# Kernel tuning notes

Hardware: AMD Instinct MI355X
Metric: run time of the kernel (lower is better)

## Reference

```python
import jax, jax.numpy as jnp
import numpy as np

N, E, H = 50000, 800000, 4
IN, HID, OUT = 128, 64, 16
SIM_THRESH = 0.1
NEG_SLOPE = 0.01  # F.leaky_relu default


def setup_inputs() -> dict:
    key = jax.random.key(0)
    k = jax.random.split(key, 6)
    x = jax.random.normal(k[0], (N, IN), jnp.float32)
    row = jax.random.randint(k[1], (E,), 0, N)
    col = jax.random.randint(k[2], (E,), 0, N)
    W0 = jax.random.normal(k[3], (H, IN, HID), jnp.float32) / np.float32(np.sqrt(IN))
    W1 = jax.random.normal(k[4], (H, H * HID, HID), jnp.float32) / np.float32(np.sqrt(H * HID))
    W2 = jax.random.normal(k[5], (1, H * HID, OUT), jnp.float32) / np.float32(np.sqrt(H * HID))
    return {"x": x, "W0": W0, "W1": W1, "W2": W2, "row": row, "col": col}


def _att_coef(x, row, col):
    # cosine similarity on edges only (honors the sparse edge structure)
    nrm = jnp.linalg.norm(x, axis=1, keepdims=True)
    xn = x / jnp.maximum(nrm, 1e-12)
    sim = jnp.sum(xn[row] * xn[col], axis=1)            # [E]
    sim = jnp.where(sim < SIM_THRESH, 0.0, sim)
    # L1 row-normalize the thresholded attention matrix
    rowsum = jax.ops.segment_sum(jnp.abs(sim), row, num_segments=N)
    rs_e = rowsum[row]
    att = jnp.where(rs_e > 0, sim / jnp.where(rs_e > 0, rs_e, 1.0), 0.0)
    # degree-based self-loop weight lam = 1/(deg+1), then exp of all nonzeros
    deg = jax.ops.segment_sum((att != 0).astype(x.dtype), row, num_segments=N)
    w_edge = jnp.where(att != 0, jnp.exp(att), 0.0)     # zero entries stay zero (dropped nnz)
    w_self = jnp.exp(1.0 / (deg + 1.0))                 # [N]
    return w_edge, w_self


def _layer(x, W, row, col, act):
    w_edge, w_self = _att_coef(x, row, col)
    z = jnp.einsum('nd,hdo->nho', x, W)                 # per-head projection
    msg = w_edge[:, None, None] * z[col]                # [E,h,o] gather + weight
    agg = jax.ops.segment_sum(msg, row, num_segments=N) + w_self[:, None, None] * z
    out = agg.reshape(N, -1)                            # concat heads (flatten(1))
    return jax.nn.leaky_relu(out, NEG_SLOPE) if act else out


def reference(x, W0, W1, W2, row, col):
    h = _layer(x, W0, row, col, True)
    h = _layer(h, W1, row, col, True)
    h = _layer(h, W2, row, col, False)
    return h
```

## Files before the change

### kernel.cpp

```cpp
#include <hip/hip_runtime.h>
#include <math.h>


static inline int cdiv(int a, int b){ return (a + b - 1) / b; }


__device__ inline float vdot(float4 a, float4 b){ return a.x*b.x + a.y*b.y + a.z*b.z + a.w*b.w; }
__device__ inline void vfma(float4& acc, float w, float4 b){
  acc.x += w*b.x; acc.y += w*b.y; acc.z += w*b.z; acc.w += w*b.w;
}
__device__ inline float4 vscale(float w, float4 a){ return make_float4(w*a.x, w*a.y, w*a.z, w*a.w); }

__device__ inline float wred(float d){
  #pragma unroll
  for (int off = 32; off; off >>= 1) d += __shfl_xor(d, off);
  return d;
}

__device__ inline unsigned short f2bf(float f){
  unsigned int u = __float_as_uint(f);
  unsigned int r = (u + 0x7FFFu + ((u >> 16) & 1u)) >> 16;
  return (unsigned short)r;
}
__device__ inline float bf2f(unsigned int us){ return __uint_as_float(us << 16); }

__device__ inline void bf8_to_f(uint4 v, float* f){
  f[0] = bf2f(v.x & 0xFFFFu); f[1] = bf2f(v.x >> 16);
  f[2] = bf2f(v.y & 0xFFFFu); f[3] = bf2f(v.y >> 16);
  f[4] = bf2f(v.z & 0xFFFFu); f[5] = bf2f(v.z >> 16);
  f[6] = bf2f(v.w & 0xFFFFu); f[7] = bf2f(v.w >> 16);
}


__global__ void count_kernel(const int* __restrict__ row, int* __restrict__ cnt, int E){
  int e = blockIdx.x * blockDim.x + threadIdx.x;
  if (e < E) atomicAdd(&cnt[row[e]], 1);
}

__global__ void scan1_kernel(const int* __restrict__ cnt, int* __restrict__ offs,
                             int* __restrict__ bsum, int n){
  __shared__ int tmp[256];
  int tid = threadIdx.x;
  int g = blockIdx.x * 256 + tid;
  int v = (g < n) ? cnt[g] : 0;
  tmp[tid] = v;
  __syncthreads();
  for (int off = 1; off < 256; off <<= 1){
    int t = (tid >= off) ? tmp[tid - off] : 0;
    __syncthreads();
    tmp[tid] += t;
    __syncthreads();
  }
  if (g < n) offs[g] = tmp[tid] - v;
  if (tid == 255) bsum[blockIdx.x] = tmp[255];
}

__global__ void scan2_kernel(int* __restrict__ bsum, int* __restrict__ offs, int nb, int n){
  __shared__ int tmp[256];
  int tid = threadIdx.x;
  int v = (tid < nb) ? bsum[tid] : 0;
  tmp[tid] = v;
  __syncthreads();
  for (int off = 1; off < 256; off <<= 1){
    int t = (tid >= off) ? tmp[tid - off] : 0;
    __syncthreads();
    tmp[tid] += t;
    __syncthreads();
  }
  if (tid < nb) bsum[tid] = tmp[tid] - v;
  if (tid == 255) offs[n] = tmp[255];
}

__global__ void scan3_kernel(int* __restrict__ offs, int* __restrict__ cur,
                             const int* __restrict__ bsum, int n){
  int g = blockIdx.x * 256 + threadIdx.x;
  if (g < n){
    int o = offs[g] + bsum[blockIdx.x];
    offs[g] = o;
    cur[g]  = o;
  }
}

__global__ void scatter_kernel(const int* __restrict__ row, const int* __restrict__ col,
                               int* __restrict__ cur, int* __restrict__ ecol, int E){
  int e = blockIdx.x * blockDim.x + threadIdx.x;
  if (e < E){
    int p = atomicAdd(&cur[row[e]], 1);
    ecol[p] = col[e];
  }
}


__global__ void invnorm128_kernel(const float* __restrict__ x, float* __restrict__ invn, int N){
  int n = blockIdx.x * 4 + (threadIdx.x >> 6);
  int lane = threadIdx.x & 63;
  if (n >= N) return;
  float2 a = ((const float2*)(x + (size_t)n * 128))[lane];
  float ss = a.x * a.x + a.y * a.y;
  ss = wred(ss);
  if (lane == 0) invn[n] = 1.0f / fmaxf(sqrtf(ss), 1e-12f);
}


template<int R>
__global__ void att_agg_wave128(const float* __restrict__ x, const float* __restrict__ invn,
                                const int* __restrict__ offs, const int* __restrict__ ecol,
                                float* __restrict__ out, int N){
  constexpr int LT = 64;
  __shared__ float tls[4][LT];
  __shared__ int   tlk[4][LT];
  const int wid  = threadIdx.x >> 6;
  const int lane = threadIdx.x & 63;
  const int half = lane >> 5, hl = lane & 31;
  const int hidx = wid * 2 + half;
  const int n = blockIdx.x * 2 + wid;
  if (n >= N) return;
  const int s = offs[n], e = offs[n + 1];
  const float inr = invn[n];
  const float4* xv = (const float4*)x;
  float4 a = xv[(size_t)n * 32 + hl];

  float4 br[R];
  float  simv[R];
  float  rowsum = 0.0f;
  int    deg = 0;

  #pragma unroll
  for (int r = 0; r < R; r++){
    simv[r] = 0.0f;
    int k = s + 2 * r + half;
    if (k < e){
      int c = ecol[k];
      float4 b = xv[(size_t)c * 32 + hl];
      br[r] = b;
      float d = vdot(a, b);
      #pragma unroll
      for (int off = 16; off; off >>= 1) d += __shfl_xor(d, off);
      d *= inr * invn[c];
      if (d < 0.1f) d = 0.0f;
      simv[r] = d;
      rowsum += d;
      deg += (d != 0.0f) ? 1 : 0;
    }
  }

  int tc = 0, kover = e;
  int k = s + 2 * R + half;
  for (; k + 2 < e; k += 4){
    int c0 = ecol[k], c1 = ecol[k + 2];
    float4 b0 = xv[(size_t)c0 * 32 + hl];
    float4 b1 = xv[(size_t)c1 * 32 + hl];
    float d0 = vdot(a, b0), d1 = vdot(a, b1);
    #pragma unroll
    for (int off = 16; off; off >>= 1){ d0 += __shfl_xor(d0, off); d1 += __shfl_xor(d1, off); }
    d0 *= inr * invn[c0];
    d1 *= inr * invn[c1];
    if (d0 < 0.1f) d0 = 0.0f;
    if (d1 < 0.1f) d1 = 0.0f;
    rowsum += d0 + d1;
    deg += (d0 != 0.0f) + (d1 != 0.0f);
    if (d0 > 0.0f){
      if (tc < LT){ if (hl == 0){ tls[hidx][tc] = d0; tlk[hidx][tc] = c0; } tc++; }
      else if (kover > k) kover = k;
    }
    if (d1 > 0.0f){
      if (tc < LT){ if (hl == 0){ tls[hidx][tc] = d1; tlk[hidx][tc] = c1; } tc++; }
      else if (kover > k + 2) kover = k + 2;
    }
  }
  if (k < e){
    int c0 = ecol[k];
    float4 b0 = xv[(size_t)c0 * 32 + hl];
    float d0 = vdot(a, b0);
    #pragma unroll
    for (int off = 16; off; off >>= 1) d0 += __shfl_xor(d0, off);
    d0 *= inr * invn[c0];
    if (d0 < 0.1f) d0 = 0.0f;
    rowsum += d0;
    deg += (d0 != 0.0f) ? 1 : 0;
    if (d0 > 0.0f){
      if (tc < LT){ if (hl == 0){ tls[hidx][tc] = d0; tlk[hidx][tc] = c0; } tc++; }
      else if (kover > k) kover = k;
    }
  }

  rowsum += __shfl_xor(rowsum, 32);
  deg    += __shfl_xor(deg, 32);
  const float invrs = (rowsum > 0.0f) ? 1.0f / rowsum : 0.0f;
  const float wself = expf(1.0f / (float)(deg + 1));

  float4 acc = (half == 0) ? vscale(wself, a) : make_float4(0.f, 0.f, 0.f, 0.f);
  #pragma unroll
  for (int r = 0; r < R; r++){
    if (simv[r] > 0.0f) vfma(acc, expf(simv[r] * invrs), br[r]);
  }
  int j = 0;
  for (; j + 1 < tc; j += 2){
    float w0 = expf(tls[hidx][j] * invrs);
    float w1 = expf(tls[hidx][j + 1] * invrs);
    int c0 = tlk[hidx][j], c1 = tlk[hidx][j + 1];
    float4 b0 = xv[(size_t)c0 * 32 + hl];
    float4 b1 = xv[(size_t)c1 * 32 + hl];
    vfma(acc, w0, b0);
    vfma(acc, w1, b1);
  }
  if (j < tc){
    float w0 = expf(tls[hidx][j] * invrs);
    float4 b0 = xv[(size_t)tlk[hidx][j] * 32 + hl];
    vfma(acc, w0, b0);
  }
  for (int k2 = kover; k2 < e; k2 += 2){
    int c = ecol[k2];
    float4 b = xv[(size_t)c * 32 + hl];
    float d = vdot(a, b);
    #pragma unroll
    for (int off = 16; off; off >>= 1) d += __shfl_xor(d, off);
    d *= inr * invn[c];
    if (d >= 0.1f) vfma(acc, expf(d * invrs), b);
  }

  acc.x += __shfl_xor(acc.x, 32);
  acc.y += __shfl_xor(acc.y, 32);
  acc.z += __shfl_xor(acc.z, 32);
  acc.w += __shfl_xor(acc.w, 32);
  if (half == 0) ((float4*)out)[(size_t)n * 32 + hl] = acc;
}


template<int R>
__global__ void att256_bf(const unsigned short* __restrict__ hbf,
                          const float* __restrict__ invn,
                          const int* __restrict__ offs, const int* __restrict__ ecol,
                          float* __restrict__ out, int N){
  constexpr int LT = 64;
  __shared__ float tls[4][LT];
  __shared__ int   tlk[4][LT];
  const int wid  = threadIdx.x >> 6;
  const int lane = threadIdx.x & 63;
  const int half = lane >> 5, hl = lane & 31;
  const int hidx = wid * 2 + half;
  const int n = blockIdx.x * 2 + wid;
  if (n >= N) return;
  const int s = offs[n], e = offs[n + 1];
  const float inr = invn[n];
  const uint4* hb = (const uint4*)hbf;

  float a8[8];
  bf8_to_f(hb[(size_t)n * 32 + hl], a8);

  uint4 brv[R];
  float simv[R];
  float rowsum = 0.0f;
  int   deg = 0;

  #pragma unroll
  for (int r = 0; r < R; r++){
    simv[r] = 0.0f;
    int k = s + 2 * r + half;
    if (k < e){
      int c = ecol[k];
      uint4 v = hb[(size_t)c * 32 + hl];
      brv[r] = v;
      float b8[8]; bf8_to_f(v, b8);
      float d = 0.0f;
      #pragma unroll
      for (int t = 0; t < 8; t++) d += a8[t] * b8[t];
      #pragma unroll
      for (int off = 16; off; off >>= 1) d += __shfl_xor(d, off);
      d *= inr * invn[c];
      if (d < 0.1f) d = 0.0f;
      simv[r] = d;
      rowsum += d;
      deg += (d != 0.0f) ? 1 : 0;
    }
  }

  int tc = 0, kover = e;
  int k = s + 2 * R + half;
  for (; k + 2 < e; k += 4){
    int c0 = ecol[k], c1 = ecol[k + 2];
    uint4 v0 = hb[(size_t)c0 * 32 + hl];
    uint4 v1 = hb[(size_t)c1 * 32 + hl];
    float b0[8], b1[8];
    bf8_to_f(v0, b0);
    bf8_to_f(v1, b1);
    float d0 = 0.0f, d1 = 0.0f;
    #pragma unroll
    for (int t = 0; t < 8; t++){ d0 += a8[t] * b0[t]; d1 += a8[t] * b1[t]; }
    #pragma unroll
    for (int off = 16; off; off >>= 1){ d0 += __shfl_xor(d0, off); d1 += __shfl_xor(d1, off); }
    d0 *= inr * invn[c0];
    d1 *= inr * invn[c1];
    if (d0 < 0.1f) d0 = 0.0f;
    if (d1 < 0.1f) d1 = 0.0f;
    rowsum += d0 + d1;
    deg += (d0 != 0.0f) + (d1 != 0.0f);
    if (d0 > 0.0f){
      if (tc < LT){ if (hl == 0){ tls[hidx][tc] = d0; tlk[hidx][tc] = c0; } tc++; }
      else if (kover > k) kover = k;
    }
    if (d1 > 0.0f){
      if (tc < LT){ if (hl == 0){ tls[hidx][tc] = d1; tlk[hidx][tc] = c1; } tc++; }
      else if (kover > k + 2) kover = k + 2;
    }
  }
  if (k < e){
    int c0 = ecol[k];
    uint4 v0 = hb[(size_t)c0 * 32 + hl];
    float b0[8]; bf8_to_f(v0, b0);
    float d0 = 0.0f;
    #pragma unroll
    for (int t = 0; t < 8; t++) d0 += a8[t] * b0[t];
    #pragma unroll
    for (int off = 16; off; off >>= 1) d0 += __shfl_xor(d0, off);
    d0 *= inr * invn[c0];
    if (d0 < 0.1f) d0 = 0.0f;
    rowsum += d0;
    deg += (d0 != 0.0f) ? 1 : 0;
    if (d0 > 0.0f){
      if (tc < LT){ if (hl == 0){ tls[hidx][tc] = d0; tlk[hidx][tc] = c0; } tc++; }
      else if (kover > k) kover = k;
    }
  }

  rowsum += __shfl_xor(rowsum, 32);
  deg    += __shfl_xor(deg, 32);
  const float invrs = (rowsum > 0.0f) ? 1.0f / rowsum : 0.0f;
  const float wself = expf(1.0f / (float)(deg + 1));

  float acc8[8];
  #pragma unroll
  for (int t = 0; t < 8; t++) acc8[t] = (half == 0) ? wself * a8[t] : 0.0f;
  #pragma unroll
  for (int r = 0; r < R; r++){
    if (simv[r] > 0.0f){
      float w = expf(simv[r] * invrs);
      float b8[8]; bf8_to_f(brv[r], b8);
      #pragma unroll
      for (int t = 0; t < 8; t++) acc8[t] += w * b8[t];
    }
  }
  int j = 0;
  for (; j + 1 < tc; j += 2){
    float w0 = expf(tls[hidx][j] * invrs);
    float w1 = expf(tls[hidx][j + 1] * invrs);
    uint4 v0 = hb[(size_t)tlk[hidx][j] * 32 + hl];
    uint4 v1 = hb[(size_t)tlk[hidx][j + 1] * 32 + hl];
    float b0[8], b1[8];
    bf8_to_f(v0, b0);
    bf8_to_f(v1, b1);
    #pragma unroll
    for (int t = 0; t < 8; t++) acc8[t] += w0 * b0[t] + w1 * b1[t];
  }
  if (j < tc){
    float w0 = expf(tls[hidx][j] * invrs);
    uint4 v0 = hb[(size_t)tlk[hidx][j] * 32 + hl];
    float b0[8]; bf8_to_f(v0, b0);
    #pragma unroll
    for (int t = 0; t < 8; t++) acc8[t] += w0 * b0[t];
  }
  for (int k2 = kover; k2 < e; k2 += 2){
    int c = ecol[k2];
    uint4 v = hb[(size_t)c * 32 + hl];
    float b[8]; bf8_to_f(v, b);
    float d = 0.0f;
    #pragma unroll
    for (int t = 0; t < 8; t++) d += a8[t] * b[t];
    #pragma unroll
    for (int off = 16; off; off >>= 1) d += __shfl_xor(d, off);
    d *= inr * invn[c];
    if (d >= 0.1f){
      float w = expf(d * invrs);
      #pragma unroll
      for (int t = 0; t < 8; t++) acc8[t] += w * b[t];
    }
  }

  #pragma unroll
  for (int t = 0; t < 8; t++) acc8[t] += __shfl_xor(acc8[t], 32);
  if (half == 0){
    float4* ov = (float4*)out;
    ov[(size_t)n * 64 + 2 * hl]     = make_float4(acc8[0], acc8[1], acc8[2], acc8[3]);
    ov[(size_t)n * 64 + 2 * hl + 1] = make_float4(acc8[4], acc8[5], acc8[6], acc8[7]);
  }
}


__global__ void att_z16_bf(const unsigned short* __restrict__ hbf,
                           const float* __restrict__ invn,
                           const int* __restrict__ offs, const int* __restrict__ ecol,
                           const float* __restrict__ z2, float* __restrict__ out, int N){
  constexpr int LT = 64;
  __shared__ float tls[4][LT];
  __shared__ int   tlk[4][LT];
  const int wid  = threadIdx.x >> 6;
  const int lane = threadIdx.x & 63;
  const int half = lane >> 5, hl = lane & 31;
  const int hidx = wid * 2 + half;
  const int n = blockIdx.x * 2 + wid;
  if (n >= N) return;
  const int s = offs[n], e = offs[n + 1];
  const float inr = invn[n];
  const uint4* hb = (const uint4*)hbf;

  float a8[8];
  bf8_to_f(hb[(size_t)n * 32 + hl], a8);

  float rowsum = 0.0f;
  int   deg = 0;
  int   tc = 0, kover = e;

  int k = s + half;
  for (; k + 2 < e; k += 4){
    int c0 = ecol[k], c1 = ecol[k + 2];
    uint4 v0 = hb[(size_t)c0 * 32 + hl];
    uint4 v1 = hb[(size_t)c1 * 32 + hl];
    float b0[8], b1[8];
    bf8_to_f(v0, b0);
    bf8_to_f(v1, b1);
    float d0 = 0.0f, d1 = 0.0f;
    #pragma unroll
    for (int t = 0; t < 8; t++){ d0 += a8[t] * b0[t]; d1 += a8[t] * b1[t]; }
    #pragma unroll
    for (int off = 16; off; off >>= 1){ d0 += __shfl_xor(d0, off); d1 += __shfl_xor(d1, off); }
    d0 *= inr * invn[c0];
    d1 *= inr * invn[c1];
    if (d0 < 0.1f) d0 = 0.0f;
    if (d1 < 0.1f) d1 = 0.0f;
    rowsum += d0 + d1;
    deg += (d0 != 0.0f) + (d1 != 0.0f);
    if (d0 > 0.0f){
      if (tc < LT){ if (hl == 0){ tls[hidx][tc] = d0; tlk[hidx][tc] = c0; } tc++; }
      else if (kover > k) kover = k;
    }
    if (d1 > 0.0f){
      if (tc < LT){ if (hl == 0){ tls[hidx][tc] = d1; tlk[hidx][tc] = c1; } tc++; }
      else if (kover > k + 2) kover = k + 2;
    }
  }
  if (k < e){
    int c0 = ecol[k];
    uint4 v0 = hb[(size_t)c0 * 32 + hl];
    float b0[8]; bf8_to_f(v0, b0);
    float d0 = 0.0f;
    #pragma unroll
    for (int t = 0; t < 8; t++) d0 += a8[t] * b0[t];
    #pragma unroll
    for (int off = 16; off; off >>= 1) d0 += __shfl_xor(d0, off);
    d0 *= inr * invn[c0];
    if (d0 < 0.1f) d0 = 0.0f;
    rowsum += d0;
    deg += (d0 != 0.0f) ? 1 : 0;
    if (d0 > 0.0f){
      if (tc < LT){ if (hl == 0){ tls[hidx][tc] = d0; tlk[hidx][tc] = c0; } tc++; }
      else if (kover > k) kover = k;
    }
  }

  rowsum += __shfl_xor(rowsum, 32);
  deg    += __shfl_xor(deg, 32);
  const float invrs = (rowsum > 0.0f) ? 1.0f / rowsum : 0.0f;
  const float wself = expf(1.0f / (float)(deg + 1));

  const int grp = hl >> 4, ch = hl & 15;
  float acc = 0.0f;
  for (int j = grp; j < tc; j += 2){
    float w = expf(tls[hidx][j] * invrs);
    int   c = tlk[hidx][j];
    acc += w * z2[(size_t)c * 16 + ch];
  }
  for (int k2 = kover; k2 < e; k2 += 2){
    int c = ecol[k2];
    uint4 v = hb[(size_t)c * 32 + hl];
    float b[8]; bf8_to_f(v, b);
    float d = 0.0f;
    #pragma unroll
    for (int t = 0; t < 8; t++) d += a8[t] * b[t];
    #pragma unroll
    for (int off = 16; off; off >>= 1) d += __shfl_xor(d, off);
    d *= inr * invn[c];
    if (d >= 0.1f){
      float w = expf(d * invrs);
      if (grp == 0) acc += w * z2[(size_t)c * 16 + ch];
    }
  }
  acc += __shfl_xor(acc, 16);
  acc += __shfl_xor(acc, 32);
  if (lane < 16) out[(size_t)n * 16 + lane] = acc + wself * z2[(size_t)n * 16 + lane];
}


template<int D>
__global__ void proj_act_norm(const float* __restrict__ xin, const float* __restrict__ W,
                              float* __restrict__ hout, float* __restrict__ invn,
                              unsigned short* __restrict__ hbf, int N){
  __shared__ float xs[16][D];
  __shared__ float red[4][16];
  int tid = threadIdx.x;
  int n0 = blockIdx.x * 16;
  for (int i = tid; i < 16 * D; i += 256){
    int nl = i / D, d = i % D;
    int n = n0 + nl;
    xs[nl][d] = (n < N) ? xin[(size_t)n * D + d] : 0.0f;
  }
  __syncthreads();
  int h = tid >> 6, o = tid & 63;
  const float* Wp = W + (size_t)h * D * 64 + o;
  float acc[16];
  #pragma unroll
  for (int i = 0; i < 16; i++) acc[i] = 0.0f;
  for (int d = 0; d < D; d++){
    float w = Wp[(size_t)d * 64];
    #pragma unroll
    for (int i = 0; i < 16; i++) acc[i] += xs[i][d] * w;
  }
  #pragma unroll
  for (int i = 0; i < 16; i++){
    float a = acc[i];
    acc[i] = (a > 0.0f) ? a : 0.01f * a;
  }
  #pragma unroll
  for (int i = 0; i < 16; i++){
    int n = n0 + i;
    if (n < N){
      hout[(size_t)n * 256 + tid] = acc[i];
      if (hbf) hbf[(size_t)n * 256 + tid] = f2bf(acc[i]);
    }
  }
  int wave = tid >> 6, lane = tid & 63;
  #pragma unroll
  for (int i = 0; i < 16; i++){
    float ss = acc[i] * acc[i];
    ss = wred(ss);
    if (lane == 0) red[wave][i] = ss;
  }
  __syncthreads();
  if (tid < 16){
    int n = n0 + tid;
    if (n < N){
      float t = red[0][tid] + red[1][tid] + red[2][tid] + red[3][tid];
      invn[n] = 1.0f / fmaxf(sqrtf(t), 1e-12f);
    }
  }
}

__global__ void proj16_kernel(const float* __restrict__ x, const float* __restrict__ W,
                              float* __restrict__ z, int N){
  __shared__ float xs[16][256];
  __shared__ float wsh[256 * 16];
  int tid = threadIdx.x;
  int n0 = blockIdx.x * 16;
  for (int i = tid; i < 16 * 256; i += 256){
    int nl = i >> 8, d = i & 255;
    int n = n0 + nl;
    xs[nl][d] = (n < N) ? x[(size_t)n * 256 + d] : 0.0f;
  }
  for (int i = tid; i < 256 * 16; i += 256) wsh[i] = W[i];
  __syncthreads();
  int nl = tid >> 4, o = tid & 15;
  float acc = 0.0f;
  for (int d = 0; d < 256; d++) acc += xs[nl][d] * wsh[d * 16 + o];
  int n = n0 + nl;
  if (n < N) z[(size_t)n * 16 + o] = acc;
}


extern "C" void kernel_launch(void* const* d_in, const int* in_sizes, int n_in,
                              void* d_out, int out_size, void* d_ws, size_t ws_size,
                              hipStream_t stream){
  const float* x  = (const float*)d_in[0];
  const float* W0 = (const float*)d_in[1];
  const float* W1 = (const float*)d_in[2];
  const float* W2 = (const float*)d_in[3];
  const int*   row = (const int*)d_in[4];
  const int*   col = (const int*)d_in[5];
  const int N = in_sizes[0] / 128;
  const int E = in_sizes[4];
  float* out = (float*)d_out;

  float* p = (float*)d_ws;
  float* hbuf   = p; p += (size_t)N * 256;
  float* aggbuf = p; p += (size_t)N * 256;
  float* z2     = p; p += (size_t)N * 16;
  float* invn   = p; p += N;
  unsigned short* hbf = (unsigned short*)p; p += (size_t)N * 128;
  int* cnt  = (int*)p;
  int* offs = cnt + N;
  int* cur  = offs + N + 1;
  int* ecol = cur + N;
  int* bsum = ecol + E;

  const int NB = cdiv(N, 256);

  hipMemsetAsync(cnt, 0, sizeof(int) * N, stream);
  count_kernel<<<cdiv(E, 256), 256, 0, stream>>>(row, cnt, E);
  scan1_kernel<<<NB, 256, 0, stream>>>(cnt, offs, bsum, N);
  scan2_kernel<<<1, 256, 0, stream>>>(bsum, offs, NB, N);
  scan3_kernel<<<NB, 256, 0, stream>>>(offs, cur, bsum, N);
  scatter_kernel<<<cdiv(E, 256), 256, 0, stream>>>(row, col, cur, ecol, E);

  invnorm128_kernel<<<cdiv(N, 4), 256, 0, stream>>>(x, invn, N);
  att_agg_wave128<8><<<cdiv(N, 2), 128, 0, stream>>>(x, invn, offs, ecol, aggbuf, N);
  proj_act_norm<128><<<cdiv(N, 16), 256, 0, stream>>>(aggbuf, W0, hbuf, invn, hbf, N);

  att256_bf<4><<<cdiv(N, 2), 128, 0, stream>>>(hbf, invn, offs, ecol, aggbuf, N);
  proj_act_norm<256><<<cdiv(N, 16), 256, 0, stream>>>(aggbuf, W1, hbuf, invn, hbf, N);

  proj16_kernel<<<cdiv(N, 16), 256, 0, stream>>>(hbuf, W2, z2, N);
  att_z16_bf<<<cdiv(N, 2), 128, 0, stream>>>(hbf, invn, offs, ecol, z2, out, N);
}
```

Before: 738.5 us.

## Retile projection kernel into 8x4 register blocks with float4 loads and stores

```diff
diff --git a/kernel.cpp b/kernel.cpp
--- a/kernel.cpp
+++ b/kernel.cpp
@@ -491,55 +491,74 @@
 
 
 template<int D>
-__global__ void proj_act_norm(const float* __restrict__ xin, const float* __restrict__ W,
-                              float* __restrict__ hout, float* __restrict__ invn,
-                              unsigned short* __restrict__ hbf, int N){
-  __shared__ float xs[16][D];
-  __shared__ float red[4][16];
-  int tid = threadIdx.x;
-  int n0 = blockIdx.x * 16;
-  for (int i = tid; i < 16 * D; i += 256){
-    int nl = i / D, d = i % D;
-    int n = n0 + nl;
-    xs[nl][d] = (n < N) ? xin[(size_t)n * D + d] : 0.0f;
+__global__ __launch_bounds__(256) void proj_act_norm(
+    const float* __restrict__ xin, const float* __restrict__ W,
+    float* __restrict__ hout, float* __restrict__ invn,
+    unsigned short* __restrict__ hbf, int N){
+  __shared__ float xs[32][D];
+  const int tid = threadIdx.x;
+  const int w = tid >> 6, l = tid & 63;
+  const int n0 = blockIdx.x * 32;
+
+  {
+    float4* xs4 = (float4*)&xs[0][0];
+    const float4* xin4 = (const float4*)(xin + (size_t)n0 * D);
+    const int rows = (N - n0 >= 32) ? 32 : (N - n0);
+    const int limit4 = rows * (D / 4);
+    constexpr int total4 = 32 * D / 4;
+    for (int i = tid; i < total4; i += 256)
+      xs4[i] = (i < limit4) ? xin4[i] : make_float4(0.f, 0.f, 0.f, 0.f);
   }
   __syncthreads();
-  int h = tid >> 6, o = tid & 63;
-  const float* Wp = W + (size_t)h * D * 64 + o;
-  float acc[16];
-  #pragma unroll
-  for (int i = 0; i < 16; i++) acc[i] = 0.0f;
-  for (int d = 0; d < D; d++){
-    float w = Wp[(size_t)d * 64];
-    #pragma unroll
-    for (int i = 0; i < 16; i++) acc[i] += xs[i][d] * w;
-  }
-  #pragma unroll
-  for (int i = 0; i < 16; i++){
-    float a = acc[i];
-    acc[i] = (a > 0.0f) ? a : 0.01f * a;
-  }
-  #pragma unroll
-  for (int i = 0; i < 16; i++){
-    int n = n0 + i;
+
+  const int h  = l >> 4;
+  const int oo = (l & 15) * 4;
+  const float* Wp = W + (size_t)h * D * 64 + oo;
+  const float* xrow = &xs[w * 8][0];
+
+  float acc[8][4];
+  #pragma unroll
+  for (int i = 0; i < 8; i++){
+    acc[i][0] = 0.f; acc[i][1] = 0.f; acc[i][2] = 0.f; acc[i][3] = 0.f;
+  }
+
+  for (int d = 0; d < D; d += 4){
+    float4 w0 = *(const float4*)(Wp + (size_t)(d + 0) * 64);
+    float4 w1 = *(const float4*)(Wp + (size_t)(d + 1) * 64);
+    float4 w2 = *(const float4*)(Wp + (size_t)(d + 2) * 64);
+    float4 w3 = *(const float4*)(Wp + (size_t)(d + 3) * 64);
+    #pragma unroll
+    for (int i = 0; i < 8; i++){
+      float4 xv = *(const float4*)(xrow + i * D + d);
+      acc[i][0] += xv.x * w0.x + xv.y * w1.x + xv.z * w2.x + xv.w * w3.x;
+      acc[i][1] += xv.x * w0.y + xv.y * w1.y + xv.z * w2.y + xv.w * w3.y;
+      acc[i][2] += xv.x * w0.z + xv.y * w1.z + xv.z * w2.z + xv.w * w3.z;
+      acc[i][3] += xv.x * w0.w + xv.y * w1.w + xv.z * w2.w + xv.w * w3.w;
+    }
+  }
+
+  const int nrow = n0 + w * 8;
+  #pragma unroll
+  for (int i = 0; i < 8; i++){
+    #pragma unroll
+    for (int j = 0; j < 4; j++){
+      float a = acc[i][j];
+      acc[i][j] = (a > 0.0f) ? a : 0.01f * a;
+    }
+    float ss = acc[i][0]*acc[i][0] + acc[i][1]*acc[i][1]
+             + acc[i][2]*acc[i][2] + acc[i][3]*acc[i][3];
+    ss = wred(ss);
+    const int n = nrow + i;
     if (n < N){
-      hout[(size_t)n * 256 + tid] = acc[i];
-      if (hbf) hbf[(size_t)n * 256 + tid] = f2bf(acc[i]);
-    }
-  }
-  int wave = tid >> 6, lane = tid & 63;
-  #pragma unroll
-  for (int i = 0; i < 16; i++){
-    float ss = acc[i] * acc[i];
-    ss = wred(ss);
-    if (lane == 0) red[wave][i] = ss;
-  }
-  __syncthreads();
-  if (tid < 16){
-    int n = n0 + tid;
-    if (n < N){
-      float t = red[0][tid] + red[1][tid] + red[2][tid] + red[3][tid];
-      invn[n] = 1.0f / fmaxf(sqrtf(t), 1e-12f);
+      if (l == 0) invn[n] = 1.0f / fmaxf(sqrtf(ss), 1e-12f);
+      ((float4*)hout)[(size_t)n * 64 + l] =
+          make_float4(acc[i][0], acc[i][1], acc[i][2], acc[i][3]);
+      if (hbf){
+        ushort4 u;
+        u.x = f2bf(acc[i][0]); u.y = f2bf(acc[i][1]);
+        u.z = f2bf(acc[i][2]); u.w = f2bf(acc[i][3]);
+        ((ushort4*)hbf)[(size_t)n * 64 + l] = u;
+      }
     }
   }
 }
@@ -601,10 +620,10 @@
 
   invnorm128_kernel<<<cdiv(N, 4), 256, 0, stream>>>(x, invn, N);
   att_agg_wave128<8><<<cdiv(N, 2), 128, 0, stream>>>(x, invn, offs, ecol, aggbuf, N);
-  proj_act_norm<128><<<cdiv(N, 16), 256, 0, stream>>>(aggbuf, W0, hbuf, invn, hbf, N);
+  proj_act_norm<128><<<cdiv(N, 32), 256, 0, stream>>>(aggbuf, W0, hbuf, invn, hbf, N);
 
   att256_bf<4><<<cdiv(N, 2), 128, 0, stream>>>(hbf, invn, offs, ecol, aggbuf, N);
-  proj_act_norm<256><<<cdiv(N, 16), 256, 0, stream>>>(aggbuf, W1, hbuf, invn, hbf, N);
+  proj_act_norm<256><<<cdiv(N, 32), 256, 0, stream>>>(aggbuf, W1, hbuf, invn, hbf, N);
 
   proj16_kernel<<<cdiv(N, 16), 256, 0, stream>>>(hbuf, W2, z2, N);
   att_z16_bf<<<cdiv(N, 2), 128, 0, stream>>>(hbf, invn, offs, ecol, z2, out, N);
```

New measurement: 667.8 us. -9.6%, faster.
